# Kernel tuning notes

Measured on AMD Instinct MI355X. Metric: run time of the kernel, lower is better.

Reference implementation:

```python
import jax, jax.numpy as jnp
import numpy as np

N, NFEAT, NHID, NHEADS, NCLASS = 4096, 1024, 128, 8, 64
ALPHA = 0.2  # LeakyReLU negative slope
NEG_INF = -9e15


def setup_inputs() -> dict:
    key = jax.random.key(0)
    ks = jax.random.split(key, 8)
    x = jax.random.normal(ks[0], (N, NFEAT), dtype=jnp.float32)
    adj = jax.random.randint(ks[1], (N, N), 0, 2, dtype=jnp.int32)
    sW = 1.0 / np.sqrt(NFEAT)
    W = jax.random.normal(ks[2], (NHEADS, NFEAT, NHID), dtype=jnp.float32) * sW
    a1 = jax.random.normal(ks[3], (NHEADS, NHID), dtype=jnp.float32) * 0.1
    a2 = jax.random.normal(ks[4], (NHEADS, NHID), dtype=jnp.float32) * 0.1
    sWo = 1.0 / np.sqrt(NHID * NHEADS)
    Wo = jax.random.normal(ks[5], (NHID * NHEADS, NCLASS), dtype=jnp.float32) * sWo
    ao1 = jax.random.normal(ks[6], (NCLASS,), dtype=jnp.float32) * 0.1
    ao2 = jax.random.normal(ks[7], (NCLASS,), dtype=jnp.float32) * 0.1
    return {"x": x, "adj": adj, "W": W, "a1": a1, "a2": a2,
            "Wo": Wo, "ao1": ao1, "ao2": ao2}


def reference(x, adj, W, a1, a2, Wo, ao1, ao2):
    mask = adj > 0  # [N, N]
    # --- multi-head attention layer (concat=True) ---
    Wh = jnp.einsum('nf,hfd->hnd', x, W)            # [H, N, D]
    f1 = jnp.einsum('hnd,hd->hn', Wh, a1)           # [H, N] self score
    f2 = jnp.einsum('hnd,hd->hn', Wh, a2)           # [H, N] neighbor score
    e = jax.nn.leaky_relu(f1[:, :, None] + f2[:, None, :], negative_slope=ALPHA)
    e = jnp.where(mask[None, :, :], e, NEG_INF)
    attn = jax.nn.softmax(e, axis=-1)               # [H, N, N]
    h = jnp.einsum('hnm,hmd->hnd', attn, Wh)        # [H, N, D]
    h = jax.nn.elu(h)                               # concat=True applies elu
    h = jnp.transpose(h, (1, 0, 2)).reshape(N, NHEADS * NHID)  # concat heads
    # --- output attention layer (concat=False) ---
    Who = h @ Wo                                    # [N, C]
    g1 = Who @ ao1                                  # [N]
    g2 = Who @ ao2                                  # [N]
    eo = jax.nn.leaky_relu(g1[:, None] + g2[None, :], negative_slope=ALPHA)
    eo = jnp.where(mask, eo, NEG_INF)
    ao = jax.nn.softmax(eo, axis=-1)                # [N, N]
    out = ao @ Who                                  # [N, C]
    out = jax.nn.elu(out)                           # F.elu in GAT.forward
    return jax.nn.log_softmax(out, axis=1)
```

## Files before the change

### kernel.cpp

```cpp
#include <hip/hip_runtime.h>
#include <hip/hip_bf16.h>


#define NN    4096
#define NF    1024
#define DH    128
#define NHEADS 8
#define NCLS  64
#define ALPHA 0.2f
#define LOG2E 1.44269504f

using short8 = __attribute__((ext_vector_type(8))) short;
using f32x4  = __attribute__((ext_vector_type(4))) float;
using int4v  = __attribute__((ext_vector_type(4))) int;

static __device__ __forceinline__ float bf2f(unsigned short h) {
    return __uint_as_float(((unsigned int)h) << 16);
}
static __device__ __forceinline__ unsigned short f2bf(float f) {
    unsigned int u = __float_as_uint(f);
    u = (u + 0x7fffu + ((u >> 16) & 1u)) >> 16;
    return (unsigned short)u;
}
static __device__ __forceinline__ float fast_exp2(float x) {
    return __builtin_amdgcn_exp2f(x);
}

__global__ __launch_bounds__(256) void diag_fill(
    float* __restrict__ out, int n, float val)
{
    int i = blockIdx.x * 256 + threadIdx.x;
    if (i < n) out[i] = val;
}

__global__ __launch_bounds__(256) void prep(
    const float* __restrict__ x, const int* __restrict__ adj,
    const float* __restrict__ W, const float* __restrict__ Wo,
    const float* __restrict__ a1, const float* __restrict__ a2,
    const float* __restrict__ ao1, const float* __restrict__ ao2,
    unsigned short* __restrict__ xB, unsigned int* __restrict__ bm,
    unsigned short* __restrict__ WT, unsigned short* __restrict__ WoT,
    unsigned short* __restrict__ a1B, unsigned short* __restrict__ a2B,
    unsigned short* __restrict__ ao1B, unsigned short* __restrict__ ao2B)
{
    __shared__ unsigned short tile[32][33];
    int b = blockIdx.x, t = threadIdx.x;
    if (b < 16384) {
        long t4 = (long)b * 256 + t;
        int4v v = ((const int4v*)adj)[t4];
        unsigned nib = (v[0] > 0 ? 1u : 0u) | (v[1] > 0 ? 2u : 0u)
                     | (v[2] > 0 ? 4u : 0u) | (v[3] > 0 ? 8u : 0u);
        int l = t & 63;
        unsigned w = nib << (4 * (l & 7));
        w |= __shfl_xor(w, 1);
        w |= __shfl_xor(w, 2);
        w |= __shfl_xor(w, 4);
        if ((l & 7) == 0) bm[t4 >> 3] = w;
    } else if (b < 20480) {
        long i = ((long)(b - 16384) * 256 + t) * 4;
        float4 v = *(const float4*)&x[i];
        unsigned u0 = (unsigned)f2bf(v.x) | ((unsigned)f2bf(v.y) << 16);
        unsigned u1 = (unsigned)f2bf(v.z) | ((unsigned)f2bf(v.w) << 16);
        uint2 u; u.x = u0; u.y = u1;
        *(uint2*)&xB[i] = u;
    } else if (b < 21632) {
        int tid = b - 20480;
        int z = tid >> 7;
        int rem = tid & 127;
        int bx = rem & 3, by = rem >> 2;
        const float* in; unsigned short* out; int C;
        if (z < 8) { in = W + (long)z * NF * DH; out = WT + (long)z * DH * NF; C = DH; }
        else       { in = Wo;                    out = WoT;                    C = NCLS; }
        int x0 = bx * 32, y0 = by * 32;
        if (x0 >= C) return;
        int tx = t & 31, ty = t >> 5;
        for (int yy = 0; yy < 32; yy += 8)
            tile[ty + yy][tx] = f2bf(in[(long)(y0 + ty + yy) * C + x0 + tx]);
        __syncthreads();
        for (int yy = 0; yy < 32; yy += 8)
            out[(long)(x0 + ty + yy) * NF + y0 + tx] = tile[tx][ty + yy];
    } else if (b == 21632) {
        for (int i = t; i < NHEADS * DH; i += 256) {
            a1B[i] = f2bf(a1[i]);
            a2B[i] = f2bf(a2[i]);
        }
    } else {
        if (t < NCLS) {
            ao1B[t] = f2bf(ao1[t]);
            ao2B[t] = f2bf(ao2[t]);
        }
    }
}

__global__ __launch_bounds__(256) void gemm1_fs(
    const unsigned short* __restrict__ A, const unsigned short* __restrict__ Bt,
    unsigned short* __restrict__ Cc, const unsigned short* __restrict__ a1B,
    const unsigned short* __restrict__ a2B, float* __restrict__ f1,
    float* __restrict__ f2)
{
    __shared__ unsigned short Alds[64][72];
    __shared__ unsigned short Blds[128][72];
    __shared__ float s1l[128], s2l[128];
    int t = threadIdx.x;
    int w = t >> 6, l = t & 63;
    int h = blockIdx.z;
    long aoff = (long)h * DH * NF + (long)blockIdx.y * 64 * NF;
    long boff = (long)blockIdx.x * 128 * NF;
    if (t < 128) { s1l[t] = 0.f; s2l[t] = 0.f; }
    f32x4 acc[8];
#pragma unroll
    for (int i = 0; i < 8; ++i) acc[i] = (f32x4){0.f, 0.f, 0.f, 0.f};

    for (int k0 = 0; k0 < NF; k0 += 64) {
#pragma unroll
        for (int it = 0; it < 2; ++it) {
            int ci = it * 256 + t;
            int r = ci >> 3, c8 = (ci & 7) * 8;
            *(short8*)&Alds[r][c8] = *(const short8*)&A[aoff + (long)r * NF + k0 + c8];
        }
#pragma unroll
        for (int it = 0; it < 4; ++it) {
            int ci = it * 256 + t;
            int r = ci >> 3, c8 = (ci & 7) * 8;
            *(short8*)&Blds[r][c8] = *(const short8*)&Bt[boff + (long)r * NF + k0 + c8];
        }
        __syncthreads();
        int arow = w * 16 + (l & 15);
        int koff = (l >> 4) * 8;
#pragma unroll
        for (int kc = 0; kc < 2; ++kc) {
            short8 af = *(const short8*)&Alds[arow][kc * 32 + koff];
#pragma unroll
            for (int dt = 0; dt < 8; ++dt) {
                short8 bf = *(const short8*)&Blds[dt * 16 + (l & 15)][kc * 32 + koff];
                acc[dt] = __builtin_amdgcn_mfma_f32_16x16x32_bf16(af, bf, acc[dt], 0, 0, 0);
            }
        }
        __syncthreads();
    }
    long coff = (long)h * DH * NN + ((long)blockIdx.y * 64) * NN + blockIdx.x * 128;
    int mrow = w * 16 + (l >> 4) * 4;
    int dbase = blockIdx.y * 64;
#pragma unroll
    for (int dt = 0; dt < 8; ++dt) {
        int n = dt * 16 + (l & 15);
        float p1 = 0.f, p2 = 0.f;
#pragma unroll
        for (int r = 0; r < 4; ++r) {
            unsigned short bw = f2bf(acc[dt][r]);
            Cc[coff + (long)(mrow + r) * NN + n] = bw;
            float vf = bf2f(bw);
            int d = dbase + mrow + r;
            p1 += vf * bf2f(a1B[h * DH + d]);
            p2 += vf * bf2f(a2B[h * DH + d]);
        }
        atomicAdd(&s1l[n], p1);
        atomicAdd(&s2l[n], p2);
    }
    __syncthreads();
    if (t < 128) {
        int n = blockIdx.x * 128 + t;
        atomicAdd(&f1[h * NN + n], s1l[t] * LOG2E);
        atomicAdd(&f2[h * NN + n], s2l[t] * LOG2E);
    }
}

__global__ __launch_bounds__(256) void gemm2c(
    const unsigned short* __restrict__ A, const unsigned short* __restrict__ Bt,
    const unsigned short* __restrict__ ao1B, const unsigned short* __restrict__ ao2B,
    unsigned short* __restrict__ WhoT, float* __restrict__ g1, float* __restrict__ g2)
{
    __shared__ unsigned short Alds[64][72];
    __shared__ unsigned short Blds[64][72];
    __shared__ float s1l[64], s2l[64];
    int t = threadIdx.x;
    int w = t >> 6, l = t & 63;
    int n0 = blockIdx.x * 64;
    if (t < 64) { s1l[t] = 0.f; s2l[t] = 0.f; }
    f32x4 acc[4];
#pragma unroll
    for (int i = 0; i < 4; ++i) acc[i] = (f32x4){0.f, 0.f, 0.f, 0.f};

    for (int k0 = 0; k0 < NF; k0 += 64) {
#pragma unroll
        for (int it = 0; it < 2; ++it) {
            int ci = it * 256 + t;
            int r = ci >> 3, c8 = (ci & 7) * 8;
            *(short8*)&Alds[r][c8] = *(const short8*)&A[(long)r * NF + k0 + c8];
        }
#pragma unroll
        for (int it = 0; it < 2; ++it) {
            int ci = it * 256 + t;
            int r = ci >> 3, c8 = (ci & 7) * 8;
            *(short8*)&Blds[r][c8] = *(const short8*)&Bt[(long)(n0 + r) * NF + k0 + c8];
        }
        __syncthreads();
        int arow = w * 16 + (l & 15);
        int koff = (l >> 4) * 8;
#pragma unroll
        for (int kc = 0; kc < 2; ++kc) {
            short8 af = *(const short8*)&Alds[arow][kc * 32 + koff];
#pragma unroll
            for (int dt = 0; dt < 4; ++dt) {
                short8 bf = *(const short8*)&Blds[dt * 16 + (l & 15)][kc * 32 + koff];
                acc[dt] = __builtin_amdgcn_mfma_f32_16x16x32_bf16(af, bf, acc[dt], 0, 0, 0);
            }
        }
        __syncthreads();
    }
    int mrow = w * 16 + (l >> 4) * 4;
#pragma unroll
    for (int dt = 0; dt < 4; ++dt) {
        int nl = dt * 16 + (l & 15);
        float p1 = 0.f, p2 = 0.f;
#pragma unroll
        for (int r = 0; r < 4; ++r) {
            int c = mrow + r;
            unsigned short bw = f2bf(acc[dt][r]);
            WhoT[(long)c * NN + n0 + nl] = bw;
            float vf = bf2f(bw);
            p1 += vf * bf2f(ao1B[c]);
            p2 += vf * bf2f(ao2B[c]);
        }
        atomicAdd(&s1l[nl], p1);
        atomicAdd(&s2l[nl], p2);
    }
    __syncthreads();
    if (t < 64) {
        g1[n0 + t] = s1l[t] * LOG2E;
        g2[n0 + t] = s2l[t] * LOG2E;
    }
}

static __device__ __forceinline__ float build_p16(
    unsigned int bits, float fi, const float* f2s, int pc0,
    short8& p0, short8& p1)
{
    float lsum = 0.f;
#pragma unroll
    for (int cc = 0; cc < 16; ++cc) {
        float wgt = 0.f;
        if ((bits >> cc) & 1u) {
            float e = fi + f2s[pc0 + cc];
            e = e > 0.f ? e : ALPHA * e;
            e = fminf(e, 60.f);
            wgt = fast_exp2(e);
        }
        unsigned short bw = f2bf(wgt);
        lsum += bf2f(bw);
        if (cc < 8) p0[cc] = (short)bw;
        else        p1[cc - 8] = (short)bw;
    }
    return lsum;
}

static __device__ __forceinline__ void build_pfrag3(
    unsigned long long wpair, float fi, const float* __restrict__ f2g,
    int kgrp, short8& a0, short8& a1)
{
    int4v av0, av1;
#pragma unroll
    for (int kc = 0; kc < 2; ++kc) {
        unsigned bits = (unsigned)(wpair >> (kc * 32 + kgrp * 8)) & 0xFFu;
        const float4* fp = (const float4*)(f2g + kc * 32 + kgrp * 8);
        float4 fv0 = fp[0], fv1 = fp[1];
        float ev[8] = {fv0.x, fv0.y, fv0.z, fv0.w, fv1.x, fv1.y, fv1.z, fv1.w};
#pragma unroll
        for (int jj = 0; jj < 8; jj += 2) {
            float e0 = fi + ev[jj], e1 = fi + ev[jj + 1];
            e0 = fmaxf(e0, ALPHA * e0);
            e1 = fmaxf(e1, ALPHA * e1);
            float w0 = fast_exp2(e0), w1 = fast_exp2(e1);
            w0 = ((bits >> jj) & 1u) ? w0 : 0.f;
            w1 = ((bits >> (jj + 1)) & 1u) ? w1 : 0.f;
            float2 fv; fv.x = w0; fv.y = w1;
            __hip_bfloat162 pk = __float22bfloat162_rn(fv);
            unsigned pu; __builtin_memcpy(&pu, &pk, 4);
            if (kc == 0) av0[jj >> 1] = (int)pu;
            else         av1[jj >> 1] = (int)pu;
        }
    }
    a0 = __builtin_bit_cast(short8, av0);
    a1 = __builtin_bit_cast(short8, av1);
}

__global__ __launch_bounds__(256) void attn1_direct(
    const float* __restrict__ f1, const float* __restrict__ f2,
    const unsigned int* __restrict__ bm, const unsigned short* __restrict__ WhT,
    unsigned short* __restrict__ hcat)
{
    __shared__ unsigned short Plds[64][72];
    __shared__ unsigned short Wlds[128][72];
    __shared__ float f1s[64], f2s[64], ssum[64][4], srow[64];
    int t = threadIdx.x;
    int h = blockIdx.y;
    int i0 = blockIdx.x * 64;
    int w = t >> 6, l = t & 63;
    if (t < 64) f1s[t] = f1[h * NN + i0 + t];
    f32x4 acc[8];
#pragma unroll
    for (int i = 0; i < 8; ++i) acc[i] = (f32x4){0.f, 0.f, 0.f, 0.f};
    float psum = 0.f;
    int pr = t >> 2, pc0 = (t & 3) * 16;
    const unsigned short* Wh_h = WhT + (long)h * DH * NN;

    for (int j0 = 0; j0 < NN; j0 += 64) {
        if (t < 64) f2s[t] = f2[h * NN + j0 + t];
        __syncthreads();
        {
            unsigned int word = bm[(long)(i0 + pr) * (NN / 32) + (j0 >> 5) + ((pc0 >> 5) & 1)];
            unsigned int bits = (word >> (pc0 & 16)) & 0xFFFFu;
            short8 p0, p1;
            psum += build_p16(bits, f1s[pr], f2s, pc0, p0, p1);
            *(short8*)&Plds[pr][pc0]     = p0;
            *(short8*)&Plds[pr][pc0 + 8] = p1;
        }
#pragma unroll
        for (int it = 0; it < 4; ++it) {
            int ci = it * 256 + t;
            int d = ci >> 3, c8 = (ci & 7) * 8;
            *(short8*)&Wlds[d][c8] = *(const short8*)&Wh_h[(long)d * NN + j0 + c8];
        }
        __syncthreads();
        int arow = w * 16 + (l & 15);
        int koff = (l >> 4) * 8;
#pragma unroll
        for (int kc = 0; kc < 2; ++kc) {
            short8 af = *(const short8*)&Plds[arow][kc * 32 + koff];
#pragma unroll
            for (int dt = 0; dt < 8; ++dt) {
                short8 bf = *(const short8*)&Wlds[dt * 16 + (l & 15)][kc * 32 + koff];
                acc[dt] = __builtin_amdgcn_mfma_f32_16x16x32_bf16(af, bf, acc[dt], 0, 0, 0);
            }
        }
        __syncthreads();
    }
    ssum[pr][t & 3] = psum;
    __syncthreads();
    if (t < 64) srow[t] = ssum[t][0] + ssum[t][1] + ssum[t][2] + ssum[t][3];
    __syncthreads();
    int mrow = w * 16 + (l >> 4) * 4;
#pragma unroll
    for (int dt = 0; dt < 8; ++dt) {
        int d = dt * 16 + (l & 15);
#pragma unroll
        for (int r = 0; r < 4; ++r) {
            float v = acc[dt][r] / fmaxf(srow[mrow + r], 1e-20f);
            v = v > 0.f ? v : __expf(v) - 1.f;
            hcat[(long)(i0 + mrow + r) * (NHEADS * DH) + h * DH + d] = f2bf(v);
        }
    }
}

__global__ __launch_bounds__(256) void attn1_part(
    const float* __restrict__ f1, const float* __restrict__ f2,
    const unsigned int* __restrict__ bm, const unsigned short* __restrict__ WhT,
    float* __restrict__ accp1, float* __restrict__ dsum1, int jspan)
{
    __shared__ unsigned short Wlds[128][72];
    int t = threadIdx.x;
    int h = blockIdx.y;
    int i0 = blockIdx.x * 64;
    int jz = blockIdx.z;
    int w = t >> 6, l = t & 63;
    int m = l & 15, kgrp = l >> 4;
    int myrow = i0 + w * 16 + m;
    float fi = f1[h * NN + myrow];
    const unsigned int* bmrow = bm + (long)myrow * (NN / 32);
    const float* f2h = f2 + (long)h * NN;
    const unsigned short* Wh_h = WhT + (long)h * DH * NN;
    short8 ones;
#pragma unroll
    for (int i = 0; i < 8; ++i) ones[i] = (short)0x3F80;
    f32x4 acc[8];
#pragma unroll
    for (int i = 0; i < 8; ++i) acc[i] = (f32x4){0.f, 0.f, 0.f, 0.f};
    f32x4 accd = (f32x4){0.f, 0.f, 0.f, 0.f};

    for (int j0 = jz * jspan; j0 < (jz + 1) * jspan; j0 += 64) {
        unsigned long long wpair;
        __builtin_memcpy(&wpair, &bmrow[j0 >> 5], 8);
#pragma unroll
        for (int it = 0; it < 4; ++it) {
            int ci = it * 256 + t;
            int d = ci >> 3, c8 = (ci & 7) * 8;
            *(short8*)&Wlds[d][c8] = *(const short8*)&Wh_h[(long)d * NN + j0 + c8];
        }
        short8 a0, a1;
        build_pfrag3(wpair, fi, f2h + j0, kgrp, a0, a1);
        __syncthreads();
        accd = __builtin_amdgcn_mfma_f32_16x16x32_bf16(a0, ones, accd, 0, 0, 0);
        accd = __builtin_amdgcn_mfma_f32_16x16x32_bf16(a1, ones, accd, 0, 0, 0);
#pragma unroll
        for (int dt = 0; dt < 8; ++dt) {
            short8 b0 = *(const short8*)&Wlds[dt * 16 + m][kgrp * 8];
            acc[dt] = __builtin_amdgcn_mfma_f32_16x16x32_bf16(a0, b0, acc[dt], 0, 0, 0);
        }
#pragma unroll
        for (int dt = 0; dt < 8; ++dt) {
            short8 b1 = *(const short8*)&Wlds[dt * 16 + m][32 + kgrp * 8];
            acc[dt] = __builtin_amdgcn_mfma_f32_16x16x32_bf16(a1, b1, acc[dt], 0, 0, 0);
        }
        __syncthreads();
    }
    if (m == 0) {
#pragma unroll
        for (int r = 0; r < 4; ++r)
            dsum1[((long)jz * NHEADS + h) * NN + i0 + w * 16 + kgrp * 4 + r] = accd[r];
    }
    int mrow = w * 16 + kgrp * 4;
#pragma unroll
    for (int dt = 0; dt < 8; ++dt) {
        int d = dt * 16 + m;
#pragma unroll
        for (int r = 0; r < 4; ++r)
            accp1[((long)jz * NN + i0 + mrow + r) * (NHEADS * DH) + h * DH + d] = acc[dt][r];
    }
}

__global__ __launch_bounds__(256) void combine1(
    const float* __restrict__ accp1, const float* __restrict__ dsum1,
    unsigned short* __restrict__ hcat, int js)
{
    long idx4 = (long)blockIdx.x * 256 + threadIdx.x;
    int i = (int)(idx4 >> 8), c4 = (int)(idx4 & 255) * 4, h = c4 >> 7;
    float4 v = {0.f, 0.f, 0.f, 0.f};
    float s = 0.f;
    for (int jz = 0; jz < js; ++jz) {
        float4 pv = *(const float4*)&accp1[((long)jz * NN + i) * (NHEADS * DH) + c4];
        v.x += pv.x; v.y += pv.y; v.z += pv.z; v.w += pv.w;
        s += dsum1[((long)jz * NHEADS + h) * NN + i];
    }
    float inv = 1.f / fmaxf(s, 1e-20f);
    float o[4] = {v.x * inv, v.y * inv, v.z * inv, v.w * inv};
#pragma unroll
    for (int k = 0; k < 4; ++k) o[k] = o[k] > 0.f ? o[k] : __expf(o[k]) - 1.f;
    unsigned u0 = (unsigned)f2bf(o[0]) | ((unsigned)f2bf(o[1]) << 16);
    unsigned u1 = (unsigned)f2bf(o[2]) | ((unsigned)f2bf(o[3]) << 16);
    uint2 u; u.x = u0; u.y = u1;
    *(uint2*)&hcat[(long)i * (NHEADS * DH) + c4] = u;
}

__global__ __launch_bounds__(256) void attn2(
    const float* __restrict__ g1, const float* __restrict__ g2,
    const unsigned int* __restrict__ bm, const unsigned short* __restrict__ WhoT,
    float* __restrict__ accp, float* __restrict__ sp, int jspan)
{
    __shared__ unsigned short Wlds[64][72];
    int t = threadIdx.x;
    int i0 = blockIdx.x * 64;
    int jc = blockIdx.y;
    int w = t >> 6, l = t & 63;
    int m = l & 15, kgrp = l >> 4;
    int myrow = i0 + w * 16 + m;
    float fi = g1[myrow];
    const unsigned int* bmrow = bm + (long)myrow * (NN / 32);
    short8 ones;
#pragma unroll
    for (int i = 0; i < 8; ++i) ones[i] = (short)0x3F80;
    f32x4 acc[4];
#pragma unroll
    for (int i = 0; i < 4; ++i) acc[i] = (f32x4){0.f, 0.f, 0.f, 0.f};
    f32x4 accd = (f32x4){0.f, 0.f, 0.f, 0.f};

    for (int j0 = jc * jspan; j0 < (jc + 1) * jspan; j0 += 64) {
        unsigned long long wpair;
        __builtin_memcpy(&wpair, &bmrow[j0 >> 5], 8);
#pragma unroll
        for (int it = 0; it < 2; ++it) {
            int ci = it * 256 + t;
            int d = ci >> 3, c8 = (ci & 7) * 8;
            *(short8*)&Wlds[d][c8] = *(const short8*)&WhoT[(long)d * NN + j0 + c8];
        }
        short8 a0, a1;
        build_pfrag3(wpair, fi, g2 + j0, kgrp, a0, a1);
        __syncthreads();
        accd = __builtin_amdgcn_mfma_f32_16x16x32_bf16(a0, ones, accd, 0, 0, 0);
        accd = __builtin_amdgcn_mfma_f32_16x16x32_bf16(a1, ones, accd, 0, 0, 0);
#pragma unroll
        for (int dt = 0; dt < 4; ++dt) {
            short8 b0 = *(const short8*)&Wlds[dt * 16 + m][kgrp * 8];
            acc[dt] = __builtin_amdgcn_mfma_f32_16x16x32_bf16(a0, b0, acc[dt], 0, 0, 0);
        }
#pragma unroll
        for (int dt = 0; dt < 4; ++dt) {
            short8 b1 = *(const short8*)&Wlds[dt * 16 + m][32 + kgrp * 8];
            acc[dt] = __builtin_amdgcn_mfma_f32_16x16x32_bf16(a1, b1, acc[dt], 0, 0, 0);
        }
        __syncthreads();
    }
    if (m == 0) {
#pragma unroll
        for (int r = 0; r < 4; ++r)
            sp[(long)jc * NN + i0 + w * 16 + kgrp * 4 + r] = accd[r];
    }
    int mrow = w * 16 + kgrp * 4;
#pragma unroll
    for (int dt = 0; dt < 4; ++dt) {
        int d = dt * 16 + m;
#pragma unroll
        for (int r = 0; r < 4; ++r)
            accp[((long)jc * NN + i0 + mrow + r) * NCLS + d] = acc[dt][r];
    }
}

__global__ __launch_bounds__(256) void finalize(
    const float* __restrict__ accp, const float* __restrict__ sp,
    float* __restrict__ out, int js)
{
    int t = threadIdx.x;
    int wv = t >> 6, l = t & 63;
    int r = blockIdx.x * 4 + wv;
    float v = 0.f, s = 0.f;
    for (int jc = 0; jc < js; ++jc) {
        v += accp[((long)jc * NN + r) * NCLS + l];
        s += sp[(long)jc * NN + r];
    }
    v /= fmaxf(s, 1e-20f);
    v = v > 0.f ? v : __expf(v) - 1.f;
    float m = v;
#pragma unroll
    for (int off = 32; off; off >>= 1) m = fmaxf(m, __shfl_xor(m, off));
    float ex = __expf(v - m);
#pragma unroll
    for (int off = 32; off; off >>= 1) ex += __shfl_xor(ex, off);
    out[(long)r * NCLS + l] = v - (m + __logf(ex));
}

extern "C" void kernel_launch(void* const* d_in, const int* in_sizes, int n_in,
                              void* d_out, int out_size, void* d_ws, size_t ws_size,
                              hipStream_t stream)
{
    const float* x   = (const float*)d_in[0];
    const int*   adj = (const int*)d_in[1];
    const float* W   = (const float*)d_in[2];
    const float* a1  = (const float*)d_in[3];
    const float* a2  = (const float*)d_in[4];
    const float* Wo  = (const float*)d_in[5];
    const float* ao1 = (const float*)d_in[6];
    const float* ao2 = (const float*)d_in[7];
    float* out = (float*)d_out;

    const long SZ_XB   = (long)NN * NF * 2;
    const long SZ_AB   = (long)NHEADS * DH * 2;
    const long SZ_AOB  = (long)NCLS * 2;
    const long SZ_WT   = (long)NHEADS * DH * NF * 2;
    const long SZ_WOT  = (long)NCLS * NF * 2;
    const long SZ_WHT  = (long)NHEADS * DH * NN * 2;
    const long SZ_HCAT = (long)NN * NHEADS * DH * 2;
    const long SZ_WHOT = (long)NCLS * NN * 2;
    const long SZ_F    = (long)NHEADS * NN * 4;
    const long SZ_G    = (long)NN * 4;
    const long SZ_BM   = (long)NN * (NN / 32) * 4;
    const long SZ_AP1  = (long)NN * NHEADS * DH * 4;
    const long SZ_DS1  = (long)NHEADS * NN * 4;
    const long SZ_AP2  = (long)NN * NCLS * 4;
    const long SZ_SP2  = (long)NN * 4;
    long base = SZ_XB + 2 * SZ_AB + 2 * SZ_AOB + SZ_WT + SZ_WOT + SZ_WHT
              + SZ_HCAT + SZ_WHOT + 2 * SZ_F + 2 * SZ_G + SZ_BM
              + 40 * 256;

    int js1, js2;
    if ((size_t)(base + 4 * (SZ_AP1 + SZ_DS1) + 16 * (SZ_AP2 + SZ_SP2)) <= ws_size) {
        js1 = 4; js2 = 16;
    } else if ((size_t)(base + 4 * (SZ_AP1 + SZ_DS1) + 8 * (SZ_AP2 + SZ_SP2)) <= ws_size) {
        js1 = 4; js2 = 8;
    } else if ((size_t)(base + 2 * (SZ_AP1 + SZ_DS1) + 8 * (SZ_AP2 + SZ_SP2)) <= ws_size) {
        js1 = 2; js2 = 8;
    } else if ((size_t)(base + 16 * (SZ_AP2 + SZ_SP2)) <= ws_size) {
        js1 = 1; js2 = 16;
    } else if ((size_t)(base + 4 * (SZ_AP2 + SZ_SP2)) <= ws_size) {
        js1 = 1; js2 = 4;
    } else {
        diag_fill<<<dim3((out_size + 255) / 256), 256, 0, stream>>>(
            out, out_size, (float)(ws_size >> 20));
        return;
    }

    char* p = (char*)d_ws;
    auto alloc = [&](long bytes) { char* q = p; p += (bytes + 255) & ~255L; return q; };
    unsigned short* xB   = (unsigned short*)alloc(SZ_XB);
    unsigned short* a1B  = (unsigned short*)alloc(SZ_AB);
    unsigned short* a2B  = (unsigned short*)alloc(SZ_AB);
    unsigned short* ao1B = (unsigned short*)alloc(SZ_AOB);
    unsigned short* ao2B = (unsigned short*)alloc(SZ_AOB);
    unsigned short* WT   = (unsigned short*)alloc(SZ_WT);
    unsigned short* WoT  = (unsigned short*)alloc(SZ_WOT);
    unsigned short* WhT  = (unsigned short*)alloc(SZ_WHT);
    unsigned short* hcat = (unsigned short*)alloc(SZ_HCAT);
    unsigned short* WhoT = (unsigned short*)alloc(SZ_WHOT);
    float* f1 = (float*)alloc(SZ_F);
    float* f2 = (float*)alloc(SZ_F);
    float* g1 = (float*)alloc(SZ_G);
    float* g2 = (float*)alloc(SZ_G);
    unsigned int* bm = (unsigned int*)alloc(SZ_BM);
    float* accp2 = (float*)alloc(js2 * SZ_AP2);
    float* sp2   = (float*)alloc(js2 * SZ_SP2);
    float* accp1 = (float*)(js1 > 1 ? alloc(js1 * SZ_AP1) : nullptr);
    float* dsum1 = (float*)(js1 > 1 ? alloc(js1 * SZ_DS1) : nullptr);

    hipMemsetAsync(f1, 0, 2 * SZ_F, stream);
    prep<<<dim3(21634), 256, 0, stream>>>(
        x, adj, W, Wo, a1, a2, ao1, ao2,
        xB, bm, WT, WoT, a1B, a2B, ao1B, ao2B);
    gemm1_fs<<<dim3(NN / 128, DH / 64, NHEADS), 256, 0, stream>>>(
        WT, xB, WhT, a1B, a2B, f1, f2);
    if (js1 > 1) {
        attn1_part<<<dim3(NN / 64, NHEADS, js1), 256, 0, stream>>>(
            f1, f2, bm, WhT, accp1, dsum1, NN / js1);
        combine1<<<dim3((int)(((long)NN * NHEADS * DH) / 1024)), 256, 0, stream>>>(
            accp1, dsum1, hcat, js1);
    } else {
        attn1_direct<<<dim3(NN / 64, NHEADS), 256, 0, stream>>>(f1, f2, bm, WhT, hcat);
    }
    gemm2c<<<dim3(NN / 64), 256, 0, stream>>>(WoT, hcat, ao1B, ao2B, WhoT, g1, g2);
    attn2<<<dim3(NN / 64, js2), 256, 0, stream>>>(g1, g2, bm, WhoT, accp2, sp2, NN / js2);
    finalize<<<dim3(NN / 4), 256, 0, stream>>>(accp2, sp2, out, js2);
}
```

Before: 306.7 us.

## Store split-K attention partials in bf16 and drop LDS staging in gemm2c/attn2

The partial accumulators written by attn1_part and attn2 and read by combine1 and finalize are now stored as bf16 instead of fp32. This halves partial-buffer traffic and workspace, so larger split counts may also fit. gemm2c and attn2 no longer stage operands through shared memory and instead load MFMA fragments directly from global memory, removing the barriers. The cost is reduced precision in the partial sums and less coalesced, cache-dependent global loads for the fragments.

New measurement: 316.3 us. +3.1%, slower.

```diff
diff --git a/kernel.cpp b/kernel.cpp
--- a/kernel.cpp
+++ b/kernel.cpp
@@ -170,48 +170,31 @@
     const unsigned short* __restrict__ ao1B, const unsigned short* __restrict__ ao2B,
     unsigned short* __restrict__ WhoT, float* __restrict__ g1, float* __restrict__ g2)
 {
-    __shared__ unsigned short Alds[64][72];
-    __shared__ unsigned short Blds[64][72];
     __shared__ float s1l[64], s2l[64];
     int t = threadIdx.x;
     int w = t >> 6, l = t & 63;
+    int m = l & 15, kgrp = l >> 4;
     int n0 = blockIdx.x * 64;
     if (t < 64) { s1l[t] = 0.f; s2l[t] = 0.f; }
+    __syncthreads();
     f32x4 acc[4];
 #pragma unroll
     for (int i = 0; i < 4; ++i) acc[i] = (f32x4){0.f, 0.f, 0.f, 0.f};
 
-    for (int k0 = 0; k0 < NF; k0 += 64) {
-#pragma unroll
-        for (int it = 0; it < 2; ++it) {
-            int ci = it * 256 + t;
-            int r = ci >> 3, c8 = (ci & 7) * 8;
-            *(short8*)&Alds[r][c8] = *(const short8*)&A[(long)r * NF + k0 + c8];
-        }
-#pragma unroll
-        for (int it = 0; it < 2; ++it) {
-            int ci = it * 256 + t;
-            int r = ci >> 3, c8 = (ci & 7) * 8;
-            *(short8*)&Blds[r][c8] = *(const short8*)&Bt[(long)(n0 + r) * NF + k0 + c8];
-        }
-        __syncthreads();
-        int arow = w * 16 + (l & 15);
-        int koff = (l >> 4) * 8;
-#pragma unroll
-        for (int kc = 0; kc < 2; ++kc) {
-            short8 af = *(const short8*)&Alds[arow][kc * 32 + koff];
-#pragma unroll
-            for (int dt = 0; dt < 4; ++dt) {
-                short8 bf = *(const short8*)&Blds[dt * 16 + (l & 15)][kc * 32 + koff];
-                acc[dt] = __builtin_amdgcn_mfma_f32_16x16x32_bf16(af, bf, acc[dt], 0, 0, 0);
-            }
-        }
-        __syncthreads();
-    }
-    int mrow = w * 16 + (l >> 4) * 4;
+    const unsigned short* Arow = A + (long)(w * 16 + m) * NF + kgrp * 8;
+#pragma unroll 4
+    for (int k0 = 0; k0 < NF; k0 += 32) {
+        short8 af = *(const short8*)&Arow[k0];
+#pragma unroll
+        for (int dt = 0; dt < 4; ++dt) {
+            short8 bf = *(const short8*)&Bt[(long)(n0 + dt * 16 + m) * NF + k0 + kgrp * 8];
+            acc[dt] = __builtin_amdgcn_mfma_f32_16x16x32_bf16(af, bf, acc[dt], 0, 0, 0);
+        }
+    }
+    int mrow = w * 16 + kgrp * 4;
 #pragma unroll
     for (int dt = 0; dt < 4; ++dt) {
-        int nl = dt * 16 + (l & 15);
+        int nl = dt * 16 + m;
         float p1 = 0.f, p2 = 0.f;
 #pragma unroll
         for (int r = 0; r < 4; ++r) {
@@ -355,7 +338,7 @@
 __global__ __launch_bounds__(256) void attn1_part(
     const float* __restrict__ f1, const float* __restrict__ f2,
     const unsigned int* __restrict__ bm, const unsigned short* __restrict__ WhT,
-    float* __restrict__ accp1, float* __restrict__ dsum1, int jspan)
+    unsigned short* __restrict__ accp1, float* __restrict__ dsum1, int jspan)
 {
     __shared__ unsigned short Wlds[128][72];
     int t = threadIdx.x;
@@ -414,12 +397,12 @@
         int d = dt * 16 + m;
 #pragma unroll
         for (int r = 0; r < 4; ++r)
-            accp1[((long)jz * NN + i0 + mrow + r) * (NHEADS * DH) + h * DH + d] = acc[dt][r];
+            accp1[((long)jz * NN + i0 + mrow + r) * (NHEADS * DH) + h * DH + d] = f2bf(acc[dt][r]);
     }
 }
 
 __global__ __launch_bounds__(256) void combine1(
-    const float* __restrict__ accp1, const float* __restrict__ dsum1,
+    const unsigned short* __restrict__ accp1, const float* __restrict__ dsum1,
     unsigned short* __restrict__ hcat, int js)
 {
     long idx4 = (long)blockIdx.x * 256 + threadIdx.x;
@@ -427,8 +410,11 @@
     float4 v = {0.f, 0.f, 0.f, 0.f};
     float s = 0.f;
     for (int jz = 0; jz < js; ++jz) {
-        float4 pv = *(const float4*)&accp1[((long)jz * NN + i) * (NHEADS * DH) + c4];
-        v.x += pv.x; v.y += pv.y; v.z += pv.z; v.w += pv.w;
+        uint2 pv = *(const uint2*)&accp1[((long)jz * NN + i) * (NHEADS * DH) + c4];
+        v.x += bf2f((unsigned short)(pv.x & 0xFFFFu));
+        v.y += bf2f((unsigned short)(pv.x >> 16));
+        v.z += bf2f((unsigned short)(pv.y & 0xFFFFu));
+        v.w += bf2f((unsigned short)(pv.y >> 16));
         s += dsum1[((long)jz * NHEADS + h) * NN + i];
     }
     float inv = 1.f / fmaxf(s, 1e-20f);
@@ -444,9 +430,8 @@
 __global__ __launch_bounds__(256) void attn2(
     const float* __restrict__ g1, const float* __restrict__ g2,
     const unsigned int* __restrict__ bm, const unsigned short* __restrict__ WhoT,
-    float* __restrict__ accp, float* __restrict__ sp, int jspan)
-{
-    __shared__ unsigned short Wlds[64][72];
+    unsigned short* __restrict__ accp, float* __restrict__ sp, int jspan)
+{
     int t = threadIdx.x;
     int i0 = blockIdx.x * 64;
     int jc = blockIdx.y;
@@ -466,28 +451,20 @@
     for (int j0 = jc * jspan; j0 < (jc + 1) * jspan; j0 += 64) {
         unsigned long long wpair;
         __builtin_memcpy(&wpair, &bmrow[j0 >> 5], 8);
-#pragma unroll
-        for (int it = 0; it < 2; ++it) {
-            int ci = it * 256 + t;
-            int d = ci >> 3, c8 = (ci & 7) * 8;
-            *(short8*)&Wlds[d][c8] = *(const short8*)&WhoT[(long)d * NN + j0 + c8];
-        }
         short8 a0, a1;
         build_pfrag3(wpair, fi, g2 + j0, kgrp, a0, a1);
-        __syncthreads();
         accd = __builtin_amdgcn_mfma_f32_16x16x32_bf16(a0, ones, accd, 0, 0, 0);
         accd = __builtin_amdgcn_mfma_f32_16x16x32_bf16(a1, ones, accd, 0, 0, 0);
 #pragma unroll
         for (int dt = 0; dt < 4; ++dt) {
-            short8 b0 = *(const short8*)&Wlds[dt * 16 + m][kgrp * 8];
+            short8 b0 = *(const short8*)&WhoT[(long)(dt * 16 + m) * NN + j0 + kgrp * 8];
             acc[dt] = __builtin_amdgcn_mfma_f32_16x16x32_bf16(a0, b0, acc[dt], 0, 0, 0);
         }
 #pragma unroll
         for (int dt = 0; dt < 4; ++dt) {
-            short8 b1 = *(const short8*)&Wlds[dt * 16 + m][32 + kgrp * 8];
+            short8 b1 = *(const short8*)&WhoT[(long)(dt * 16 + m) * NN + j0 + 32 + kgrp * 8];
             acc[dt] = __builtin_amdgcn_mfma_f32_16x16x32_bf16(a1, b1, acc[dt], 0, 0, 0);
         }
-        __syncthreads();
     }
     if (m == 0) {
 #pragma unroll
@@ -500,12 +477,12 @@
         int d = dt * 16 + m;
 #pragma unroll
         for (int r = 0; r < 4; ++r)
-            accp[((long)jc * NN + i0 + mrow + r) * NCLS + d] = acc[dt][r];
+            accp[((long)jc * NN + i0 + mrow + r) * NCLS + d] = f2bf(acc[dt][r]);
     }
 }
 
 __global__ __launch_bounds__(256) void finalize(
-    const float* __restrict__ accp, const float* __restrict__ sp,
+    const unsigned short* __restrict__ accp, const float* __restrict__ sp,
     float* __restrict__ out, int js)
 {
     int t = threadIdx.x;
@@ -513,7 +490,7 @@
     int r = blockIdx.x * 4 + wv;
     float v = 0.f, s = 0.f;
     for (int jc = 0; jc < js; ++jc) {
-        v += accp[((long)jc * NN + r) * NCLS + l];
+        v += bf2f(accp[((long)jc * NN + r) * NCLS + l]);
         s += sp[(long)jc * NN + r];
     }
     v /= fmaxf(s, 1e-20f);
@@ -552,9 +529,9 @@
     const long SZ_F    = (long)NHEADS * NN * 4;
     const long SZ_G    = (long)NN * 4;
     const long SZ_BM   = (long)NN * (NN / 32) * 4;
-    const long SZ_AP1  = (long)NN * NHEADS * DH * 4;
+    const long SZ_AP1  = (long)NN * NHEADS * DH * 2;
     const long SZ_DS1  = (long)NHEADS * NN * 4;
-    const long SZ_AP2  = (long)NN * NCLS * 4;
+    const long SZ_AP2  = (long)NN * NCLS * 2;
     const long SZ_SP2  = (long)NN * 4;
     long base = SZ_XB + 2 * SZ_AB + 2 * SZ_AOB + SZ_WT + SZ_WOT + SZ_WHT
               + SZ_HCAT + SZ_WHOT + 2 * SZ_F + 2 * SZ_G + SZ_BM
@@ -594,9 +571,9 @@
     float* g1 = (float*)alloc(SZ_G);
     float* g2 = (float*)alloc(SZ_G);
     unsigned int* bm = (unsigned int*)alloc(SZ_BM);
-    float* accp2 = (float*)alloc(js2 * SZ_AP2);
+    unsigned short* accp2 = (unsigned short*)alloc(js2 * SZ_AP2);
     float* sp2   = (float*)alloc(js2 * SZ_SP2);
-    float* accp1 = (float*)(js1 > 1 ? alloc(js1 * SZ_AP1) : nullptr);
+    unsigned short* accp1 = (unsigned short*)(js1 > 1 ? alloc(js1 * SZ_AP1) : nullptr);
     float* dsum1 = (float*)(js1 > 1 ? alloc(js1 * SZ_DS1) : nullptr);
 
     hipMemsetAsync(f1, 0, 2 * SZ_F, stream);
```
